# Optimization experiments

Measured on AMD Instinct MI355X. Metric: run time of the kernel, lower is better.

Reference implementation:

```python
import jax, jax.numpy as jnp
import numpy as np

N_NODES = 50000
N_EDGES = 500000
D_FEAT = 128
HIDDEN = 128
EPS = 1e-8


def _lin_init(key, fan_in, fan_out):
    return jax.random.normal(key, (fan_in, fan_out), dtype=jnp.float32) / np.sqrt(fan_in)


def setup_inputs() -> dict:
    key = jax.random.key(0)
    ks = jax.random.split(key, 16)
    h = jax.random.normal(ks[0], (N_NODES, D_FEAT), dtype=jnp.float32)
    coord = jax.random.normal(ks[1], (N_NODES, 3), dtype=jnp.float32)
    vel = jax.random.normal(ks[2], (N_NODES, 3), dtype=jnp.float32)
    edge_index = jax.random.randint(ks[3], (2, N_EDGES), 0, N_NODES, dtype=jnp.int32)
    return {
        "h": h, "coord": coord, "vel": vel, "edge_index": edge_index,
        "W_e1": _lin_init(ks[4], 2 * D_FEAT + 1, HIDDEN), "b_e1": jnp.zeros((HIDDEN,), jnp.float32),
        "W_e2": _lin_init(ks[5], HIDDEN, D_FEAT), "b_e2": jnp.zeros((D_FEAT,), jnp.float32),
        "W_c1": _lin_init(ks[6], D_FEAT, HIDDEN), "b_c1": jnp.zeros((HIDDEN,), jnp.float32),
        "W_c2": _lin_init(ks[7], HIDDEN, 1), "b_c2": jnp.zeros((1,), jnp.float32),
        "W_v1": _lin_init(ks[8], D_FEAT, HIDDEN), "b_v1": jnp.zeros((HIDDEN,), jnp.float32),
        "W_v2": _lin_init(ks[9], HIDDEN, 1), "b_v2": jnp.zeros((1,), jnp.float32),
        "W_n1": _lin_init(ks[10], 2 * D_FEAT, HIDDEN), "b_n1": jnp.zeros((HIDDEN,), jnp.float32),
        "W_n2": _lin_init(ks[11], HIDDEN, D_FEAT), "b_n2": jnp.zeros((D_FEAT,), jnp.float32),
    }


def reference(h, coord, vel, edge_index,
              W_e1, b_e1, W_e2, b_e2,
              W_c1, b_c1, W_c2, b_c2,
              W_v1, b_v1, W_v2, b_v2,
              W_n1, b_n1, W_n2, b_n2):
    act = jax.nn.silu
    r, c = edge_index[0], edge_index[1]
    n = coord.shape[0]

    # coord2radial with normalize=True
    diff = coord[r] - coord[c]                      # [E, 3]
    rad = jnp.sum(diff * diff, axis=-1, keepdims=True)  # [E, 1]
    norm = jnp.sqrt(jax.lax.stop_gradient(rad)) + EPS
    diff = diff / norm

    # edge_op: Linear -> act -> Linear -> act
    edge_in = jnp.concatenate([h[r], h[c], rad], axis=1)  # [E, 2D+1]
    m_ij = act(act(edge_in @ W_e1 + b_e1) @ W_e2 + b_e2)  # [E, D]

    # coord_op: Linear -> act -> Linear (scalar weight per edge)
    weights = act(m_ij @ W_c1 + b_c1) @ W_c2 + b_c2       # [E, 1]
    coors_sum = jax.ops.segment_sum(diff * weights, r, num_segments=n)  # [N, 3]

    # vel_op: Linear -> act -> Linear (scalar per node)
    vel_weights = act(h @ W_v1 + b_v1) @ W_v2 + b_v2      # [N, 1]
    coord_out = coord + coors_sum + vel * vel_weights

    # node aggregation + node_op: Linear -> act -> Linear
    m_i = jax.ops.segment_sum(m_ij, r, num_segments=h.shape[0])  # [N, D]
    agg = jnp.concatenate([h, m_i], axis=1)               # [N, 2D]
    h_out = act(agg @ W_n1 + b_n1) @ W_n2 + b_n2          # [N, D]
    return (h_out, coord_out)
```

## Files before the change

kernel.cpp:

```cpp
#include <hip/hip_runtime.h>
#include <stdint.h>

#define NN 50000
#define NE 500000
#define BLK 256
#define NEB ((NE + 127) / 128)
#define SST 136

#define BARRIER() asm volatile("s_waitcnt lgkmcnt(0)\n\ts_barrier" ::: "memory")

typedef __attribute__((ext_vector_type(8))) short bf16x8;
typedef __attribute__((ext_vector_type(4))) float f32x4;

__device__ __forceinline__ float silu(float x) { return x / (1.0f + __expf(-x)); }
__device__ __forceinline__ float bf2f(unsigned short s) {
    union { unsigned int u; float f; } v; v.u = ((unsigned int)s) << 16; return v.f;
}
__device__ __forceinline__ unsigned short f2bf(float f) {
    union { float f; unsigned int u; } v; v.f = f;
    return (unsigned short)((v.u + 0x7fffu + ((v.u >> 16) & 1u)) >> 16);
}
__device__ __forceinline__ unsigned int pack2(float a, float b) {
    unsigned int r;
    asm("v_cvt_pk_bf16_f32 %0, %1, %2" : "=v"(r) : "v"(a), "v"(b));
    return r;
}
__device__ __forceinline__ bf16x8 packf8(const float* p) {
    float4 f0 = *(const float4*)p; float4 f1 = *(const float4*)(p + 4);
    union { bf16x8 v; unsigned int u[4]; } o;
    o.u[0] = pack2(f0.x, f0.y); o.u[1] = pack2(f0.z, f0.w);
    o.u[2] = pack2(f1.x, f1.y); o.u[3] = pack2(f1.z, f1.w);
    return o.v;
}

__global__ void prep_h(const float* __restrict__ h, unsigned short* __restrict__ hb) {
    int i = blockIdx.x * 256 + threadIdx.x;
    if (i < NN * 128 / 4) {
        float4 v = ((const float4*)h)[i];
        uint2 o; o.x = pack2(v.x, v.y); o.y = pack2(v.z, v.w);
        ((uint2*)hb)[i] = o;
    }
}

__global__ void prep_w(const float* __restrict__ We1, const float* __restrict__ We2,
                       const float* __restrict__ Wc1, const float* __restrict__ Wv1,
                       const float* __restrict__ Wn1, const float* __restrict__ Wn2,
                       unsigned short* __restrict__ Wt1, unsigned short* __restrict__ Wt2,
                       unsigned short* __restrict__ Wt3, unsigned short* __restrict__ Wv1t,
                       unsigned short* __restrict__ Wn1t, unsigned short* __restrict__ Wn2t) {
    int i = blockIdx.x * 256 + threadIdx.x;
    if (i < 32768) {
        int j = i >> 8, k = i & 255;
        Wt1[i] = f2bf(We1[k * 128 + j]);
    } else if (i < 49152) {
        int t = i - 32768; int j = t >> 7, ks = t & 127;
        int k0 = (ks & 7) * 16 + (ks >> 3);
        Wt2[t] = f2bf(We2[k0 * 128 + j]);
    } else if (i < 65536) {
        int t = i - 49152; int j = t >> 7, ks = t & 127;
        int k0 = (ks & 7) * 16 + (ks >> 3);
        Wt3[t] = f2bf(Wc1[k0 * 128 + j]);
    } else if (i < 81920) {
        int t = i - 65536; int j = t >> 7, k = t & 127;
        Wv1t[t] = f2bf(Wv1[k * 128 + j]);
    } else if (i < 114688) {
        int t = i - 81920; int j = t >> 8, k = t & 255;
        int ksrc;
        if (k < 128) ksrc = k;
        else { int ks = k - 128; ksrc = 128 + (ks & 7) * 16 + (ks >> 3); }
        Wn1t[t] = f2bf(Wn1[ksrc * 128 + j]);
    } else if (i < 131072) {
        int t = i - 114688; int j = t >> 7, ks = t & 127;
        int k0 = (ks & 7) * 16 + (ks >> 3);
        Wn2t[t] = f2bf(Wn2[k0 * 128 + j]);
    }
}

__global__ void csr_count(const int* __restrict__ eidx, int* __restrict__ deg) {
    int e = blockIdx.x * 256 + threadIdx.x;
    if (e < NE) atomicAdd(&deg[eidx[e]], 1);
}

__global__ void scan_a(const int* __restrict__ deg, int* __restrict__ bsum) {
    __shared__ int s[256];
    int t = threadIdx.x, idx = blockIdx.x * 256 + t;
    s[t] = (idx < NN) ? deg[idx] : 0;
    __syncthreads();
    for (int off = 128; off > 0; off >>= 1) {
        if (t < off) s[t] += s[t + off];
        __syncthreads();
    }
    if (t == 0) bsum[blockIdx.x] = s[0];
}

__global__ void scan_b(int* __restrict__ bsum) {
    __shared__ int s[256];
    int t = threadIdx.x;
    int v = (t < 196) ? bsum[t] : 0;
    s[t] = v;
    __syncthreads();
    for (int off = 1; off < 256; off <<= 1) {
        int x = (t >= off) ? s[t - off] : 0;
        __syncthreads();
        s[t] += x;
        __syncthreads();
    }
    if (t < 196) bsum[t] = s[t] - v;
}

__global__ void scan_c(const int* __restrict__ deg, const int* __restrict__ bsum,
                       int* __restrict__ rowptr) {
    __shared__ int s[256];
    int t = threadIdx.x, idx = blockIdx.x * 256 + t;
    int v = (idx < NN) ? deg[idx] : 0;
    s[t] = v;
    __syncthreads();
    for (int off = 1; off < 256; off <<= 1) {
        int x = (t >= off) ? s[t - off] : 0;
        __syncthreads();
        s[t] += x;
        __syncthreads();
    }
    if (idx < NN) rowptr[idx] = bsum[blockIdx.x] + s[t] - v;
    if (idx == 0) rowptr[NN] = NE;
}

__global__ void csr_fill(const int* __restrict__ eidx, const int* __restrict__ rowptr,
                         int* __restrict__ cursor,
                         int* __restrict__ csr_r, int* __restrict__ csr_c) {
    int e = blockIdx.x * 256 + threadIdx.x;
    if (e < NE) {
        int r = eidx[e], c = eidx[NE + e];
        int slot = rowptr[r] + atomicAdd(&cursor[r], 1);
        csr_r[slot] = r; csr_c[slot] = c;
    }
}

__device__ __forceinline__ void wpref256(const unsigned short* __restrict__ W, int halfk,
                                         uint4 w[8], int tid) {
#pragma unroll
    for (int t = 0; t < 8; ++t) {
        int idx = tid + t * 256; int j = idx >> 4, g = idx & 15;
        w[t] = *(const uint4*)(W + (size_t)j * 256 + halfk * 128 + g * 8);
    }
}
__device__ __forceinline__ void wpref128(const unsigned short* __restrict__ W,
                                         uint4 w[8], int tid) {
#pragma unroll
    for (int t = 0; t < 8; ++t) {
        int idx = tid + t * 256; int j = idx >> 4, g = idx & 15;
        w[t] = *(const uint4*)(W + (size_t)j * 128 + g * 8);
    }
}
__device__ __forceinline__ void wwrite(const uint4 w[8], unsigned short* sW, int tid) {
#pragma unroll
    for (int t = 0; t < 8; ++t) {
        int idx = tid + t * 256; int j = idx >> 4, g = idx & 15;
        *(uint4*)(sW + j * SST + g * 8) = w[t];
    }
}
__device__ __forceinline__ void mfma4(const bf16x8 a[2][4], const unsigned short* sW,
                                      int l16, int q, f32x4 acc[2][8]) {
#pragma unroll
    for (int kc = 0; kc < 4; ++kc)
#pragma unroll
        for (int ct = 0; ct < 8; ++ct) {
            bf16x8 b = *(const bf16x8*)(sW + (ct * 16 + l16) * SST + kc * 32 + q * 8);
            acc[0][ct] = __builtin_amdgcn_mfma_f32_16x16x32_bf16(a[0][kc], b, acc[0][ct], 0, 0, 0);
            acc[1][ct] = __builtin_amdgcn_mfma_f32_16x16x32_bf16(a[1][kc], b, acc[1][ct], 0, 0, 0);
        }
}

__global__ __launch_bounds__(BLK, 2) void egcl_edge(
    const float* __restrict__ coord,
    const int* __restrict__ csr_r, const int* __restrict__ csr_c,
    const unsigned short* __restrict__ hb,
    const unsigned short* __restrict__ Wt1,
    const unsigned short* __restrict__ Wt2,
    const unsigned short* __restrict__ Wt3,
    const float* __restrict__ We1,
    const float* __restrict__ be1, const float* __restrict__ be2,
    const float* __restrict__ bc1,
    const float* __restrict__ Wc2, const float* __restrict__ bc2,
    float* __restrict__ m_acc, float* __restrict__ c_sum)
{
    __shared__ __align__(16) unsigned short sAb[128 * SST];
    __shared__ __align__(16) unsigned short sW[128 * SST];
    __shared__ float sRad[128], sDif[128][3];
    __shared__ int sSeg[128];
    __shared__ float sBe1[128], sBe2[128], sBc1[128], sWlast[128], sWc2f[128];

    const int tid = threadIdx.x;
    const int wv = tid >> 6, lane = tid & 63, q = lane >> 4, l16 = lane & 15;
    const int e0 = blockIdx.x * 128;

    int nr[2], nc[2];
#pragma unroll
    for (int si = 0; si < 2; ++si) {
        int e = e0 + (wv * 2 + si) * 16 + l16;
        if (e >= NE) e = NE - 1;
        nr[si] = csr_r[e]; nc[si] = csr_c[e];
    }

    if (tid < 128) {
        sBe1[tid] = be1[tid]; sBe2[tid] = be2[tid]; sBc1[tid] = bc1[tid];
        sWlast[tid] = We1[256 * 128 + tid]; sWc2f[tid] = Wc2[tid];
        int s = e0 + tid; int sc = (s < NE) ? s : (NE - 1);
        int r = csr_r[sc], c = csr_c[sc];
        sSeg[tid] = (s < NE) ? r : -1;
        float dx = coord[r * 3 + 0] - coord[c * 3 + 0];
        float dy = coord[r * 3 + 1] - coord[c * 3 + 1];
        float dz = coord[r * 3 + 2] - coord[c * 3 + 2];
        float rad = fmaf(dx, dx, fmaf(dy, dy, dz * dz));
        float inv = 1.0f / (sqrtf(rad) + 1e-8f);
        sRad[tid] = rad;
        sDif[tid][0] = dx * inv; sDif[tid][1] = dy * inv; sDif[tid][2] = dz * inv;
    }

    uint4 wA[8], wB[8];
    wpref256(Wt1, 0, wA, tid);
    wpref256(Wt1, 1, wB, tid);
    bf16x8 ar[2][4], ac[2][4];
#pragma unroll
    for (int si = 0; si < 2; ++si)
#pragma unroll
        for (int kc = 0; kc < 4; ++kc) {
            ar[si][kc] = *(const bf16x8*)(hb + (size_t)nr[si] * 128 + kc * 32 + q * 8);
            ac[si][kc] = *(const bf16x8*)(hb + (size_t)nc[si] * 128 + kc * 32 + q * 8);
        }
    wwrite(wA, sW, tid);
    wwrite(wB, sAb, tid);
    wpref128(Wt2, wA, tid);
    const float bc2v = bc2[0];
    BARRIER();

    f32x4 acc[2][8];
#pragma unroll
    for (int si = 0; si < 2; ++si)
#pragma unroll
        for (int ct = 0; ct < 8; ++ct) acc[si][ct] = (f32x4){0.f, 0.f, 0.f, 0.f};

    mfma4(ar, sW, l16, q, acc);
    mfma4(ac, sAb, l16, q, acc);
    BARRIER();
    wwrite(wA, sW, tid);
    wpref128(Wt3, wA, tid);

#pragma unroll
    for (int si = 0; si < 2; ++si)
#pragma unroll
        for (int r = 0; r < 4; ++r) {
            int row = (wv * 2 + si) * 16 + q * 4 + r;
            float rad = sRad[row];
            float v[8];
#pragma unroll
            for (int ct = 0; ct < 8; ++ct) {
                int col = ct * 16 + l16;
                v[ct] = silu(acc[si][ct][r] + rad * sWlast[col] + sBe1[col]);
            }
            uint4 pk = make_uint4(pack2(v[0], v[1]), pack2(v[2], v[3]),
                                  pack2(v[4], v[5]), pack2(v[6], v[7]));
            *(uint4*)(sAb + row * SST + l16 * 8) = pk;
        }
    BARRIER();

#pragma unroll
    for (int si = 0; si < 2; ++si)
#pragma unroll
        for (int ct = 0; ct < 8; ++ct) acc[si][ct] = (f32x4){0.f, 0.f, 0.f, 0.f};
    {
        bf16x8 a[2][4];
#pragma unroll
        for (int si = 0; si < 2; ++si) {
            int row = (wv * 2 + si) * 16 + l16;
#pragma unroll
            for (int kc = 0; kc < 4; ++kc)
                a[si][kc] = *(const bf16x8*)(sAb + row * SST + kc * 32 + q * 8);
        }
        mfma4(a, sW, l16, q, acc);
    }
#pragma unroll
    for (int si = 0; si < 2; ++si)
#pragma unroll
        for (int r = 0; r < 4; ++r) {
            float v[8];
#pragma unroll
            for (int ct = 0; ct < 8; ++ct) v[ct] = silu(acc[si][ct][r] + sBe2[ct * 16 + l16]);
            int row = (wv * 2 + si) * 16 + q * 4 + r;
            *(uint4*)(sAb + row * SST + l16 * 8) =
                make_uint4(pack2(v[0], v[1]), pack2(v[2], v[3]),
                           pack2(v[4], v[5]), pack2(v[6], v[7]));
        }
    BARRIER();
    wwrite(wA, sW, tid);
    BARRIER();

#pragma unroll
    for (int si = 0; si < 2; ++si)
#pragma unroll
        for (int ct = 0; ct < 8; ++ct) acc[si][ct] = (f32x4){0.f, 0.f, 0.f, 0.f};
    {
        bf16x8 a[2][4];
#pragma unroll
        for (int si = 0; si < 2; ++si) {
            int row = (wv * 2 + si) * 16 + l16;
#pragma unroll
            for (int kc = 0; kc < 4; ++kc)
                a[si][kc] = *(const bf16x8*)(sAb + row * SST + kc * 32 + q * 8);
        }
        mfma4(a, sW, l16, q, acc);
    }
#pragma unroll
    for (int si = 0; si < 2; ++si) {
        float p[4];
#pragma unroll
        for (int r = 0; r < 4; ++r) {
            float s = 0.f;
#pragma unroll
            for (int ct = 0; ct < 8; ++ct) {
                int col = ct * 16 + l16;
                float t = silu(acc[si][ct][r] + sBc1[col]);
                s = fmaf(t, sWc2f[col], s);
            }
            p[r] = s;
        }
#pragma unroll
        for (int m = 1; m < 16; m <<= 1)
#pragma unroll
            for (int r = 0; r < 4; ++r) p[r] += __shfl_xor(p[r], m, 16);
        if (l16 == 0) {
#pragma unroll
            for (int r = 0; r < 4; ++r) {
                int row = (wv * 2 + si) * 16 + q * 4 + r;
                int rn = sSeg[row];
                if (rn >= 0) {
                    float wgt = p[r] + bc2v;
                    atomicAdd(&c_sum[(size_t)rn * 3 + 0], sDif[row][0] * wgt);
                    atomicAdd(&c_sum[(size_t)rn * 3 + 1], sDif[row][1] * wgt);
                    atomicAdd(&c_sum[(size_t)rn * 3 + 2], sDif[row][2] * wgt);
                }
            }
        }
    }

    {
        int p = tid & 127, half = tid >> 7;
        int base = half * 64;
        float run = 0.f;
        int cur = sSeg[base];
        bool openL = true;
#pragma unroll 1
        for (int i0 = 0; i0 < 64; i0 += 4) {
            float v[4]; int rr[4];
#pragma unroll
            for (int j = 0; j < 4; ++j) {
                int row = base + i0 + j;
                rr[j] = sSeg[row];
                v[j] = bf2f(sAb[row * SST + p]);
            }
#pragma unroll
            for (int j = 0; j < 4; ++j) {
                if (rr[j] != cur) {
                    if (cur >= 0) {
                        float* dst = &m_acc[(size_t)cur * 128 + p];
                        if (openL) atomicAdd(dst, run);
                        else       *dst = run;
                    }
                    run = 0.f; cur = rr[j]; openL = false;
                }
                run += v[j];
            }
        }
        if (cur >= 0) atomicAdd(&m_acc[(size_t)cur * 128 + p], run);
    }
}

__global__ __launch_bounds__(BLK, 3) void egcl_node(
    const unsigned short* __restrict__ hb,
    const float* __restrict__ coord,
    const float* __restrict__ vel,
    const unsigned short* __restrict__ Wv1t, const float* __restrict__ bv1,
    const float* __restrict__ Wv2, const float* __restrict__ bv2,
    const unsigned short* __restrict__ Wn1t, const float* __restrict__ bn1,
    const unsigned short* __restrict__ Wn2t, const float* __restrict__ bn2,
    const float* __restrict__ m_acc, const float* __restrict__ c_sum,
    float* __restrict__ out_h, float* __restrict__ out_c)
{
    __shared__ __align__(16) unsigned short sAb[128 * SST];
    __shared__ float sBv1[128], sWv2f[128], sBn1[128], sBn2[128];

    const int tid = threadIdx.x;
    const int wv = tid >> 6, lane = tid & 63, q = lane >> 4, l16 = lane & 15;
    const int n0 = blockIdx.x * 128;
    int nval = NN - n0; if (nval > 128) nval = 128;

    if (tid < 128) {
        sBv1[tid] = bv1[tid]; sWv2f[tid] = Wv2[tid];
        sBn1[tid] = bn1[tid]; sBn2[tid] = bn2[tid];
    }
    const float bv2v = bv2[0];

    bf16x8 ah[2][4], am[2][4];
#pragma unroll
    for (int si = 0; si < 2; ++si) {
        int row = (wv * 2 + si) * 16 + l16;
        int nn = n0 + row; if (nn >= NN) nn = NN - 1;
#pragma unroll
        for (int kc = 0; kc < 4; ++kc) {
            ah[si][kc] = *(const bf16x8*)(hb + (size_t)nn * 128 + kc * 32 + q * 8);
            am[si][kc] = packf8(m_acc + (size_t)nn * 128 + kc * 32 + q * 8);
        }
    }

    BARRIER();

    f32x4 acc[2][8];
#pragma unroll
    for (int si = 0; si < 2; ++si)
#pragma unroll
        for (int ct = 0; ct < 8; ++ct) acc[si][ct] = (f32x4){0.f, 0.f, 0.f, 0.f};
#pragma unroll
    for (int kc = 0; kc < 4; ++kc)
#pragma unroll
        for (int ct = 0; ct < 8; ++ct) {
            bf16x8 b = *(const bf16x8*)(Wv1t + (size_t)(ct * 16 + l16) * 128 + kc * 32 + q * 8);
            acc[0][ct] = __builtin_amdgcn_mfma_f32_16x16x32_bf16(ah[0][kc], b, acc[0][ct], 0, 0, 0);
            acc[1][ct] = __builtin_amdgcn_mfma_f32_16x16x32_bf16(ah[1][kc], b, acc[1][ct], 0, 0, 0);
        }
#pragma unroll
    for (int si = 0; si < 2; ++si) {
        float p[4];
#pragma unroll
        for (int r = 0; r < 4; ++r) {
            float s = 0.f;
#pragma unroll
            for (int ct = 0; ct < 8; ++ct) {
                int col = ct * 16 + l16;
                float t = silu(acc[si][ct][r] + sBv1[col]);
                s = fmaf(t, sWv2f[col], s);
            }
            p[r] = s;
        }
#pragma unroll
        for (int m = 1; m < 16; m <<= 1)
#pragma unroll
            for (int r = 0; r < 4; ++r) p[r] += __shfl_xor(p[r], m, 16);
        if (l16 == 0) {
#pragma unroll
            for (int r = 0; r < 4; ++r) {
                int row = (wv * 2 + si) * 16 + q * 4 + r;
                int n = n0 + row;
                if (row < nval) {
                    float vw = p[r] + bv2v;
#pragma unroll
                    for (int d = 0; d < 3; ++d) {
                        float cv = coord[(size_t)n * 3 + d] + c_sum[(size_t)n * 3 + d]
                                 + vel[(size_t)n * 3 + d] * vw;
                        out_c[(size_t)n * 3 + d] = cv;
                    }
                }
            }
        }
    }

#pragma unroll
    for (int si = 0; si < 2; ++si)
#pragma unroll
        for (int ct = 0; ct < 8; ++ct) acc[si][ct] = (f32x4){0.f, 0.f, 0.f, 0.f};
#pragma unroll
    for (int kc = 0; kc < 8; ++kc)
#pragma unroll
        for (int ct = 0; ct < 8; ++ct) {
            bf16x8 b = *(const bf16x8*)(Wn1t + (size_t)(ct * 16 + l16) * 256 + kc * 32 + q * 8);
            bf16x8 a0 = (kc < 4) ? ah[0][kc & 3] : am[0][kc & 3];
            bf16x8 a1 = (kc < 4) ? ah[1][kc & 3] : am[1][kc & 3];
            acc[0][ct] = __builtin_amdgcn_mfma_f32_16x16x32_bf16(a0, b, acc[0][ct], 0, 0, 0);
            acc[1][ct] = __builtin_amdgcn_mfma_f32_16x16x32_bf16(a1, b, acc[1][ct], 0, 0, 0);
        }
#pragma unroll
    for (int si = 0; si < 2; ++si)
#pragma unroll
        for (int r = 0; r < 4; ++r) {
            int row = (wv * 2 + si) * 16 + q * 4 + r;
            float v[8];
#pragma unroll
            for (int ct = 0; ct < 8; ++ct) v[ct] = silu(acc[si][ct][r] + sBn1[ct * 16 + l16]);
            uint4 pk = make_uint4(pack2(v[0], v[1]), pack2(v[2], v[3]),
                                  pack2(v[4], v[5]), pack2(v[6], v[7]));
            *(uint4*)(sAb + row * SST + l16 * 8) = pk;
        }

    BARRIER();

#pragma unroll
    for (int si = 0; si < 2; ++si)
#pragma unroll
        for (int ct = 0; ct < 8; ++ct) acc[si][ct] = (f32x4){0.f, 0.f, 0.f, 0.f};
    {
        bf16x8 a[2][4];
#pragma unroll
        for (int si = 0; si < 2; ++si) {
            int row = (wv * 2 + si) * 16 + l16;
#pragma unroll
            for (int kc = 0; kc < 4; ++kc)
                a[si][kc] = *(const bf16x8*)(sAb + row * SST + kc * 32 + q * 8);
        }
#pragma unroll
        for (int kc = 0; kc < 4; ++kc)
#pragma unroll
            for (int ct = 0; ct < 8; ++ct) {
                bf16x8 b = *(const bf16x8*)(Wn2t + (size_t)(ct * 16 + l16) * 128 + kc * 32 + q * 8);
                acc[0][ct] = __builtin_amdgcn_mfma_f32_16x16x32_bf16(a[0][kc], b, acc[0][ct], 0, 0, 0);
                acc[1][ct] = __builtin_amdgcn_mfma_f32_16x16x32_bf16(a[1][kc], b, acc[1][ct], 0, 0, 0);
            }
    }
#pragma unroll
    for (int si = 0; si < 2; ++si)
#pragma unroll
        for (int r = 0; r < 4; ++r) {
            int row = (wv * 2 + si) * 16 + q * 4 + r;
            if (row < nval) {
                float* orow = out_h + (size_t)(n0 + row) * 128;
#pragma unroll
                for (int ct = 0; ct < 8; ++ct)
                    orow[ct * 16 + l16] = acc[si][ct][r] + sBn2[ct * 16 + l16];
            }
        }
}

extern "C" void kernel_launch(void* const* d_in, const int* in_sizes, int n_in,
                              void* d_out, int out_size, void* d_ws, size_t ws_size,
                              hipStream_t stream) {
    const float* h     = (const float*)d_in[0];
    const float* coord = (const float*)d_in[1];
    const float* vel   = (const float*)d_in[2];
    const int*   eidx  = (const int*)d_in[3];
    const float* We1 = (const float*)d_in[4];
    const float* be1 = (const float*)d_in[5];
    const float* We2 = (const float*)d_in[6];
    const float* be2 = (const float*)d_in[7];
    const float* Wc1 = (const float*)d_in[8];
    const float* bc1 = (const float*)d_in[9];
    const float* Wc2 = (const float*)d_in[10];
    const float* bc2 = (const float*)d_in[11];
    const float* Wv1 = (const float*)d_in[12];
    const float* bv1 = (const float*)d_in[13];
    const float* Wv2 = (const float*)d_in[14];
    const float* bv2 = (const float*)d_in[15];
    const float* Wn1 = (const float*)d_in[16];
    const float* bn1 = (const float*)d_in[17];
    const float* Wn2 = (const float*)d_in[18];
    const float* bn2 = (const float*)d_in[19];

    char* ws = (char*)d_ws;
    float* m_acc = (float*)ws;
    float* c_sum = (float*)(ws + 25600000);
    unsigned short* hb   = (unsigned short*)(ws + 26200064);
    unsigned short* Wt1  = (unsigned short*)(ws + 39000064);
    unsigned short* Wt2  = (unsigned short*)(ws + 39065600);
    unsigned short* Wt3  = (unsigned short*)(ws + 39098368);
    unsigned short* Wv1t = (unsigned short*)(ws + 39131136);
    unsigned short* Wn1t = (unsigned short*)(ws + 39163904);
    unsigned short* Wn2t = (unsigned short*)(ws + 39229440);
    int* deg    = (int*)(ws + 39262208);
    int* cursor = (int*)(ws + 39462208);
    int* rowptr = (int*)(ws + 39662208);
    int* bsum   = (int*)(ws + 39862272);
    int* csr_r  = (int*)(ws + 39863296);
    int* csr_c  = (int*)(ws + 41863296);

    hipMemsetAsync(ws, 0, 26200000, stream);
    hipMemsetAsync(ws + 39262208, 0, 400000, stream);

    prep_h<<<6250, 256, 0, stream>>>(h, hb);
    prep_w<<<512, 256, 0, stream>>>(We1, We2, Wc1, Wv1, Wn1, Wn2,
                                    Wt1, Wt2, Wt3, Wv1t, Wn1t, Wn2t);

    csr_count<<<1954, 256, 0, stream>>>(eidx, deg);
    scan_a<<<196, 256, 0, stream>>>(deg, bsum);
    scan_b<<<1, 256, 0, stream>>>(bsum);
    scan_c<<<196, 256, 0, stream>>>(deg, bsum, rowptr);
    csr_fill<<<1954, 256, 0, stream>>>(eidx, rowptr, cursor, csr_r, csr_c);

    egcl_edge<<<NEB, BLK, 0, stream>>>(
        coord, csr_r, csr_c, hb, Wt1, Wt2, Wt3,
        We1, be1, be2, bc1, Wc2, bc2, m_acc, c_sum);

    float* out_h = (float*)d_out;
    float* out_c = out_h + (size_t)NN * 128;
    egcl_node<<<(NN + 127) / 128, BLK, 0, stream>>>(
        hb, coord, vel, Wv1t, bv1, Wv2, bv2, Wn1t, bn1, Wn2t, bn2,
        m_acc, c_sum, out_h, out_c);
}
```

Measured before the change: 414.5 us.

## Fuse prep kernels, reuse degree counters, and halve per-wave tiles in edge/node kernels

Merges the h conversion, weight transposition, degree counting and workspace zeroing into one prep launch, replacing two memsets and three kernels. The cursor array goes away because csr_fill now decrements the degree counters to assign slots. The edge kernel moves to 512-thread blocks where each wave handles 16 edges instead of 32, and the node kernel uses 64-node tiles; both cut register use so more waves fit per CU. The node kernel also drops a block barrier in favour of an LDS wait, which is safe only because each wave reads back just its own rows. Trade-offs: more weight-staging traffic per edge, and a reversed slot order within each CSR row.

Result: slower. 427.3 us (+3.1%).

```diff
diff --git a/kernel.cpp b/kernel.cpp
--- a/kernel.cpp
+++ b/kernel.cpp
@@ -3,11 +3,12 @@
 
 #define NN 50000
 #define NE 500000
-#define BLK 256
+#define EBLK 512
 #define NEB ((NE + 127) / 128)
 #define SST 136
 
 #define BARRIER() asm volatile("s_waitcnt lgkmcnt(0)\n\ts_barrier" ::: "memory")
+#define LGKM0() asm volatile("s_waitcnt lgkmcnt(0)" ::: "memory")
 
 typedef __attribute__((ext_vector_type(8))) short bf16x8;
 typedef __attribute__((ext_vector_type(4))) float f32x4;
@@ -33,52 +34,55 @@
     return o.v;
 }
 
-__global__ void prep_h(const float* __restrict__ h, unsigned short* __restrict__ hb) {
-    int i = blockIdx.x * 256 + threadIdx.x;
-    if (i < NN * 128 / 4) {
+__global__ void prep_all(const float* __restrict__ h, unsigned short* __restrict__ hb,
+                         const float* __restrict__ We1, const float* __restrict__ We2,
+                         const float* __restrict__ Wc1, const float* __restrict__ Wv1,
+                         const float* __restrict__ Wn1, const float* __restrict__ Wn2,
+                         unsigned short* __restrict__ Wt1, unsigned short* __restrict__ Wt2,
+                         unsigned short* __restrict__ Wt3, unsigned short* __restrict__ Wv1t,
+                         unsigned short* __restrict__ Wn1t, unsigned short* __restrict__ Wn2t,
+                         const int* __restrict__ eidx, int* __restrict__ deg,
+                         float4* __restrict__ zbase) {
+    int b = blockIdx.x, tid = threadIdx.x;
+    if (b < 6250) {
+        int i = b * 256 + tid;
         float4 v = ((const float4*)h)[i];
         uint2 o; o.x = pack2(v.x, v.y); o.y = pack2(v.z, v.w);
         ((uint2*)hb)[i] = o;
-    }
-}
-
-__global__ void prep_w(const float* __restrict__ We1, const float* __restrict__ We2,
-                       const float* __restrict__ Wc1, const float* __restrict__ Wv1,
-                       const float* __restrict__ Wn1, const float* __restrict__ Wn2,
-                       unsigned short* __restrict__ Wt1, unsigned short* __restrict__ Wt2,
-                       unsigned short* __restrict__ Wt3, unsigned short* __restrict__ Wv1t,
-                       unsigned short* __restrict__ Wn1t, unsigned short* __restrict__ Wn2t) {
-    int i = blockIdx.x * 256 + threadIdx.x;
-    if (i < 32768) {
-        int j = i >> 8, k = i & 255;
-        Wt1[i] = f2bf(We1[k * 128 + j]);
-    } else if (i < 49152) {
-        int t = i - 32768; int j = t >> 7, ks = t & 127;
-        int k0 = (ks & 7) * 16 + (ks >> 3);
-        Wt2[t] = f2bf(We2[k0 * 128 + j]);
-    } else if (i < 65536) {
-        int t = i - 49152; int j = t >> 7, ks = t & 127;
-        int k0 = (ks & 7) * 16 + (ks >> 3);
-        Wt3[t] = f2bf(Wc1[k0 * 128 + j]);
-    } else if (i < 81920) {
-        int t = i - 65536; int j = t >> 7, k = t & 127;
-        Wv1t[t] = f2bf(Wv1[k * 128 + j]);
-    } else if (i < 114688) {
-        int t = i - 81920; int j = t >> 8, k = t & 255;
-        int ksrc;
-        if (k < 128) ksrc = k;
-        else { int ks = k - 128; ksrc = 128 + (ks & 7) * 16 + (ks >> 3); }
-        Wn1t[t] = f2bf(Wn1[ksrc * 128 + j]);
-    } else if (i < 131072) {
-        int t = i - 114688; int j = t >> 7, ks = t & 127;
-        int k0 = (ks & 7) * 16 + (ks >> 3);
-        Wn2t[t] = f2bf(Wn2[k0 * 128 + j]);
-    }
-}
-
-__global__ void csr_count(const int* __restrict__ eidx, int* __restrict__ deg) {
-    int e = blockIdx.x * 256 + threadIdx.x;
-    if (e < NE) atomicAdd(&deg[eidx[e]], 1);
+    } else if (b < 6762) {
+        int i = (b - 6250) * 256 + tid;
+        if (i < 32768) {
+            int j = i >> 8, k = i & 255;
+            Wt1[i] = f2bf(We1[k * 128 + j]);
+        } else if (i < 49152) {
+            int t = i - 32768; int j = t >> 7, ks = t & 127;
+            int k0 = (ks & 7) * 16 + (ks >> 3);
+            Wt2[t] = f2bf(We2[k0 * 128 + j]);
+        } else if (i < 65536) {
+            int t = i - 49152; int j = t >> 7, ks = t & 127;
+            int k0 = (ks & 7) * 16 + (ks >> 3);
+            Wt3[t] = f2bf(Wc1[k0 * 128 + j]);
+        } else if (i < 81920) {
+            int t = i - 65536; int j = t >> 7, k = t & 127;
+            Wv1t[t] = f2bf(Wv1[k * 128 + j]);
+        } else if (i < 114688) {
+            int t = i - 81920; int j = t >> 8, k = t & 255;
+            int ksrc;
+            if (k < 128) ksrc = k;
+            else { int ks = k - 128; ksrc = 128 + (ks & 7) * 16 + (ks >> 3); }
+            Wn1t[t] = f2bf(Wn1[ksrc * 128 + j]);
+        } else if (i < 131072) {
+            int t = i - 114688; int j = t >> 7, ks = t & 127;
+            int k0 = (ks & 7) * 16 + (ks >> 3);
+            Wn2t[t] = f2bf(Wn2[k0 * 128 + j]);
+        }
+    } else if (b < 8716) {
+        int e = (b - 6762) * 256 + tid;
+        if (e < NE) atomicAdd(&deg[eidx[e]], 1);
+    } else {
+        int i = (b - 8716) * 256 + tid;
+        if (i < 1637500) zbase[i] = make_float4(0.f, 0.f, 0.f, 0.f);
+    }
 }
 
 __global__ void scan_a(const int* __restrict__ deg, int* __restrict__ bsum) {
@@ -126,52 +130,51 @@
 }
 
 __global__ void csr_fill(const int* __restrict__ eidx, const int* __restrict__ rowptr,
-                         int* __restrict__ cursor,
+                         int* __restrict__ deg,
                          int* __restrict__ csr_r, int* __restrict__ csr_c) {
     int e = blockIdx.x * 256 + threadIdx.x;
     if (e < NE) {
         int r = eidx[e], c = eidx[NE + e];
-        int slot = rowptr[r] + atomicAdd(&cursor[r], 1);
+        int slot = rowptr[r] + atomicSub(&deg[r], 1) - 1;
         csr_r[slot] = r; csr_c[slot] = c;
     }
 }
 
 __device__ __forceinline__ void wpref256(const unsigned short* __restrict__ W, int halfk,
-                                         uint4 w[8], int tid) {
-#pragma unroll
-    for (int t = 0; t < 8; ++t) {
-        int idx = tid + t * 256; int j = idx >> 4, g = idx & 15;
+                                         uint4 w[4], int tid) {
+#pragma unroll
+    for (int t = 0; t < 4; ++t) {
+        int idx = tid + t * 512; int j = idx >> 4, g = idx & 15;
         w[t] = *(const uint4*)(W + (size_t)j * 256 + halfk * 128 + g * 8);
     }
 }
 __device__ __forceinline__ void wpref128(const unsigned short* __restrict__ W,
-                                         uint4 w[8], int tid) {
-#pragma unroll
-    for (int t = 0; t < 8; ++t) {
-        int idx = tid + t * 256; int j = idx >> 4, g = idx & 15;
+                                         uint4 w[4], int tid) {
+#pragma unroll
+    for (int t = 0; t < 4; ++t) {
+        int idx = tid + t * 512; int j = idx >> 4, g = idx & 15;
         w[t] = *(const uint4*)(W + (size_t)j * 128 + g * 8);
     }
 }
-__device__ __forceinline__ void wwrite(const uint4 w[8], unsigned short* sW, int tid) {
-#pragma unroll
-    for (int t = 0; t < 8; ++t) {
-        int idx = tid + t * 256; int j = idx >> 4, g = idx & 15;
+__device__ __forceinline__ void wwrite(const uint4 w[4], unsigned short* sW, int tid) {
+#pragma unroll
+    for (int t = 0; t < 4; ++t) {
+        int idx = tid + t * 512; int j = idx >> 4, g = idx & 15;
         *(uint4*)(sW + j * SST + g * 8) = w[t];
     }
 }
-__device__ __forceinline__ void mfma4(const bf16x8 a[2][4], const unsigned short* sW,
-                                      int l16, int q, f32x4 acc[2][8]) {
+__device__ __forceinline__ void mfma4(const bf16x8 a[4], const unsigned short* sW,
+                                      int l16, int q, f32x4 acc[8]) {
 #pragma unroll
     for (int kc = 0; kc < 4; ++kc)
 #pragma unroll
         for (int ct = 0; ct < 8; ++ct) {
             bf16x8 b = *(const bf16x8*)(sW + (ct * 16 + l16) * SST + kc * 32 + q * 8);
-            acc[0][ct] = __builtin_amdgcn_mfma_f32_16x16x32_bf16(a[0][kc], b, acc[0][ct], 0, 0, 0);
-            acc[1][ct] = __builtin_amdgcn_mfma_f32_16x16x32_bf16(a[1][kc], b, acc[1][ct], 0, 0, 0);
-        }
-}
-
-__global__ __launch_bounds__(BLK, 2) void egcl_edge(
+            acc[ct] = __builtin_amdgcn_mfma_f32_16x16x32_bf16(a[kc], b, acc[ct], 0, 0, 0);
+        }
+}
+
+__global__ __launch_bounds__(EBLK, 4) void egcl_edge(
     const float* __restrict__ coord,
     const int* __restrict__ csr_r, const int* __restrict__ csr_c,
     const unsigned short* __restrict__ hb,
@@ -194,13 +197,9 @@
     const int wv = tid >> 6, lane = tid & 63, q = lane >> 4, l16 = lane & 15;
     const int e0 = blockIdx.x * 128;
 
-    int nr[2], nc[2];
-#pragma unroll
-    for (int si = 0; si < 2; ++si) {
-        int e = e0 + (wv * 2 + si) * 16 + l16;
-        if (e >= NE) e = NE - 1;
-        nr[si] = csr_r[e]; nc[si] = csr_c[e];
-    }
+    int er = e0 + wv * 16 + l16;
+    if (er >= NE) er = NE - 1;
+    const int nr = csr_r[er], nc = csr_c[er];
 
     if (tid < 128) {
         sBe1[tid] = be1[tid]; sBe2[tid] = be2[tid]; sBc1[tid] = bc1[tid];
@@ -217,28 +216,24 @@
         sDif[tid][0] = dx * inv; sDif[tid][1] = dy * inv; sDif[tid][2] = dz * inv;
     }
 
-    uint4 wA[8], wB[8];
+    uint4 wA[4], wB[4];
     wpref256(Wt1, 0, wA, tid);
     wpref256(Wt1, 1, wB, tid);
-    bf16x8 ar[2][4], ac[2][4];
-#pragma unroll
-    for (int si = 0; si < 2; ++si)
-#pragma unroll
-        for (int kc = 0; kc < 4; ++kc) {
-            ar[si][kc] = *(const bf16x8*)(hb + (size_t)nr[si] * 128 + kc * 32 + q * 8);
-            ac[si][kc] = *(const bf16x8*)(hb + (size_t)nc[si] * 128 + kc * 32 + q * 8);
-        }
+    bf16x8 ar[4], ac[4];
+#pragma unroll
+    for (int kc = 0; kc < 4; ++kc) {
+        ar[kc] = *(const bf16x8*)(hb + (size_t)nr * 128 + kc * 32 + q * 8);
+        ac[kc] = *(const bf16x8*)(hb + (size_t)nc * 128 + kc * 32 + q * 8);
+    }
     wwrite(wA, sW, tid);
     wwrite(wB, sAb, tid);
     wpref128(Wt2, wA, tid);
     const float bc2v = bc2[0];
     BARRIER();
 
-    f32x4 acc[2][8];
-#pragma unroll
-    for (int si = 0; si < 2; ++si)
-#pragma unroll
-        for (int ct = 0; ct < 8; ++ct) acc[si][ct] = (f32x4){0.f, 0.f, 0.f, 0.f};
+    f32x4 acc[8];
+#pragma unroll
+    for (int ct = 0; ct < 8; ++ct) acc[ct] = (f32x4){0.f, 0.f, 0.f, 0.f};
 
     mfma4(ar, sW, l16, q, acc);
     mfma4(ac, sAb, l16, q, acc);
@@ -247,71 +242,56 @@
     wpref128(Wt3, wA, tid);
 
 #pragma unroll
-    for (int si = 0; si < 2; ++si)
-#pragma unroll
-        for (int r = 0; r < 4; ++r) {
-            int row = (wv * 2 + si) * 16 + q * 4 + r;
-            float rad = sRad[row];
-            float v[8];
-#pragma unroll
-            for (int ct = 0; ct < 8; ++ct) {
-                int col = ct * 16 + l16;
-                v[ct] = silu(acc[si][ct][r] + rad * sWlast[col] + sBe1[col]);
-            }
-            uint4 pk = make_uint4(pack2(v[0], v[1]), pack2(v[2], v[3]),
-                                  pack2(v[4], v[5]), pack2(v[6], v[7]));
-            *(uint4*)(sAb + row * SST + l16 * 8) = pk;
-        }
+    for (int r = 0; r < 4; ++r) {
+        int row = wv * 16 + q * 4 + r;
+        float rad = sRad[row];
+        float v[8];
+#pragma unroll
+        for (int ct = 0; ct < 8; ++ct) {
+            int col = ct * 16 + l16;
+            v[ct] = silu(acc[ct][r] + rad * sWlast[col] + sBe1[col]);
+        }
+        uint4 pk = make_uint4(pack2(v[0], v[1]), pack2(v[2], v[3]),
+                              pack2(v[4], v[5]), pack2(v[6], v[7]));
+        *(uint4*)(sAb + row * SST + l16 * 8) = pk;
+    }
     BARRIER();
 
 #pragma unroll
-    for (int si = 0; si < 2; ++si)
-#pragma unroll
-        for (int ct = 0; ct < 8; ++ct) acc[si][ct] = (f32x4){0.f, 0.f, 0.f, 0.f};
+    for (int ct = 0; ct < 8; ++ct) acc[ct] = (f32x4){0.f, 0.f, 0.f, 0.f};
     {
-        bf16x8 a[2][4];
-#pragma unroll
-        for (int si = 0; si < 2; ++si) {
-            int row = (wv * 2 + si) * 16 + l16;
-#pragma unroll
-            for (int kc = 0; kc < 4; ++kc)
-                a[si][kc] = *(const bf16x8*)(sAb + row * SST + kc * 32 + q * 8);
-        }
+        bf16x8 a[4];
+        int row = wv * 16 + l16;
+#pragma unroll
+        for (int kc = 0; kc < 4; ++kc)
+            a[kc] = *(const bf16x8*)(sAb + row * SST + kc * 32 + q * 8);
         mfma4(a, sW, l16, q, acc);
     }
 #pragma unroll
-    for (int si = 0; si < 2; ++si)
-#pragma unroll
-        for (int r = 0; r < 4; ++r) {
-            float v[8];
-#pragma unroll
-            for (int ct = 0; ct < 8; ++ct) v[ct] = silu(acc[si][ct][r] + sBe2[ct * 16 + l16]);
-            int row = (wv * 2 + si) * 16 + q * 4 + r;
-            *(uint4*)(sAb + row * SST + l16 * 8) =
-                make_uint4(pack2(v[0], v[1]), pack2(v[2], v[3]),
-                           pack2(v[4], v[5]), pack2(v[6], v[7]));
-        }
+    for (int r = 0; r < 4; ++r) {
+        float v[8];
+#pragma unroll
+        for (int ct = 0; ct < 8; ++ct) v[ct] = silu(acc[ct][r] + sBe2[ct * 16 + l16]);
+        int row = wv * 16 + q * 4 + r;
+        *(uint4*)(sAb + row * SST + l16 * 8) =
+            make_uint4(pack2(v[0], v[1]), pack2(v[2], v[3]),
+                       pack2(v[4], v[5]), pack2(v[6], v[7]));
+    }
     BARRIER();
     wwrite(wA, sW, tid);
     BARRIER();
 
 #pragma unroll
-    for (int si = 0; si < 2; ++si)
-#pragma unroll
-        for (int ct = 0; ct < 8; ++ct) acc[si][ct] = (f32x4){0.f, 0.f, 0.f, 0.f};
+    for (int ct = 0; ct < 8; ++ct) acc[ct] = (f32x4){0.f, 0.f, 0.f, 0.f};
     {
-        bf16x8 a[2][4];
-#pragma unroll
-        for (int si = 0; si < 2; ++si) {
-            int row = (wv * 2 + si) * 16 + l16;
-#pragma unroll
-            for (int kc = 0; kc < 4; ++kc)
-                a[si][kc] = *(const bf16x8*)(sAb + row * SST + kc * 32 + q * 8);
-        }
+        bf16x8 a[4];
+        int row = wv * 16 + l16;
+#pragma unroll
+        for (int kc = 0; kc < 4; ++kc)
+            a[kc] = *(const bf16x8*)(sAb + row * SST + kc * 32 + q * 8);
         mfma4(a, sW, l16, q, acc);
     }
-#pragma unroll
-    for (int si = 0; si < 2; ++si) {
+    {
         float p[4];
 #pragma unroll
         for (int r = 0; r < 4; ++r) {
@@ -319,7 +299,7 @@
 #pragma unroll
             for (int ct = 0; ct < 8; ++ct) {
                 int col = ct * 16 + l16;
-                float t = silu(acc[si][ct][r] + sBc1[col]);
+                float t = silu(acc[ct][r] + sBc1[col]);
                 s = fmaf(t, sWc2f[col], s);
             }
             p[r] = s;
@@ -331,7 +311,7 @@
         if (l16 == 0) {
 #pragma unroll
             for (int r = 0; r < 4; ++r) {
-                int row = (wv * 2 + si) * 16 + q * 4 + r;
+                int row = wv * 16 + q * 4 + r;
                 int rn = sSeg[row];
                 if (rn >= 0) {
                     float wgt = p[r] + bc2v;
@@ -343,7 +323,7 @@
         }
     }
 
-    {
+    if (tid < 256) {
         int p = tid & 127, half = tid >> 7;
         int base = half * 64;
         float run = 0.f;
@@ -375,7 +355,7 @@
     }
 }
 
-__global__ __launch_bounds__(BLK, 3) void egcl_node(
+__global__ __launch_bounds__(256, 4) void egcl_node(
     const unsigned short* __restrict__ hb,
     const float* __restrict__ coord,
     const float* __restrict__ vel,
@@ -386,13 +366,13 @@
     const float* __restrict__ m_acc, const float* __restrict__ c_sum,
     float* __restrict__ out_h, float* __restrict__ out_c)
 {
-    __shared__ __align__(16) unsigned short sAb[128 * SST];
+    __shared__ __align__(16) unsigned short sAb[64 * SST];
     __shared__ float sBv1[128], sWv2f[128], sBn1[128], sBn2[128];
 
     const int tid = threadIdx.x;
     const int wv = tid >> 6, lane = tid & 63, q = lane >> 4, l16 = lane & 15;
-    const int n0 = blockIdx.x * 128;
-    int nval = NN - n0; if (nval > 128) nval = 128;
+    const int n0 = blockIdx.x * 64;
+    int nval = NN - n0; if (nval > 64) nval = 64;
 
     if (tid < 128) {
         sBv1[tid] = bv1[tid]; sWv2f[tid] = Wv2[tid];
@@ -400,35 +380,30 @@
     }
     const float bv2v = bv2[0];
 
-    bf16x8 ah[2][4], am[2][4];
-#pragma unroll
-    for (int si = 0; si < 2; ++si) {
-        int row = (wv * 2 + si) * 16 + l16;
+    bf16x8 ah[4], am[4];
+    {
+        int row = wv * 16 + l16;
         int nn = n0 + row; if (nn >= NN) nn = NN - 1;
 #pragma unroll
         for (int kc = 0; kc < 4; ++kc) {
-            ah[si][kc] = *(const bf16x8*)(hb + (size_t)nn * 128 + kc * 32 + q * 8);
-            am[si][kc] = packf8(m_acc + (size_t)nn * 128 + kc * 32 + q * 8);
+            ah[kc] = *(const bf16x8*)(hb + (size_t)nn * 128 + kc * 32 + q * 8);
+            am[kc] = packf8(m_acc + (size_t)nn * 128 + kc * 32 + q * 8);
         }
     }
 
     BARRIER();
 
-    f32x4 acc[2][8];
-#pragma unroll
-    for (int si = 0; si < 2; ++si)
-#pragma unroll
-        for (int ct = 0; ct < 8; ++ct) acc[si][ct] = (f32x4){0.f, 0.f, 0.f, 0.f};
+    f32x4 acc[8];
+#pragma unroll
+    for (int ct = 0; ct < 8; ++ct) acc[ct] = (f32x4){0.f, 0.f, 0.f, 0.f};
 #pragma unroll
     for (int kc = 0; kc < 4; ++kc)
 #pragma unroll
         for (int ct = 0; ct < 8; ++ct) {
             bf16x8 b = *(const bf16x8*)(Wv1t + (size_t)(ct * 16 + l16) * 128 + kc * 32 + q * 8);
-            acc[0][ct] = __builtin_amdgcn_mfma_f32_16x16x32_bf16(ah[0][kc], b, acc[0][ct], 0, 0, 0);
-            acc[1][ct] = __builtin_amdgcn_mfma_f32_16x16x32_bf16(ah[1][kc], b, acc[1][ct], 0, 0, 0);
-        }
-#pragma unroll
-    for (int si = 0; si < 2; ++si) {
+            acc[ct] = __builtin_amdgcn_mfma_f32_16x16x32_bf16(ah[kc], b, acc[ct], 0, 0, 0);
+        }
+    {
         float p[4];
 #pragma unroll
         for (int r = 0; r < 4; ++r) {
@@ -436,7 +411,7 @@
 #pragma unroll
             for (int ct = 0; ct < 8; ++ct) {
                 int col = ct * 16 + l16;
-                float t = silu(acc[si][ct][r] + sBv1[col]);
+                float t = silu(acc[ct][r] + sBv1[col]);
                 s = fmaf(t, sWv2f[col], s);
             }
             p[r] = s;
@@ -448,7 +423,7 @@
         if (l16 == 0) {
 #pragma unroll
             for (int r = 0; r < 4; ++r) {
-                int row = (wv * 2 + si) * 16 + q * 4 + r;
+                int row = wv * 16 + q * 4 + r;
                 int n = n0 + row;
                 if (row < nval) {
                     float vw = p[r] + bv2v;
@@ -464,68 +439,53 @@
     }
 
 #pragma unroll
-    for (int si = 0; si < 2; ++si)
-#pragma unroll
-        for (int ct = 0; ct < 8; ++ct) acc[si][ct] = (f32x4){0.f, 0.f, 0.f, 0.f};
+    for (int ct = 0; ct < 8; ++ct) acc[ct] = (f32x4){0.f, 0.f, 0.f, 0.f};
 #pragma unroll
     for (int kc = 0; kc < 8; ++kc)
 #pragma unroll
         for (int ct = 0; ct < 8; ++ct) {
             bf16x8 b = *(const bf16x8*)(Wn1t + (size_t)(ct * 16 + l16) * 256 + kc * 32 + q * 8);
-            bf16x8 a0 = (kc < 4) ? ah[0][kc & 3] : am[0][kc & 3];
-            bf16x8 a1 = (kc < 4) ? ah[1][kc & 3] : am[1][kc & 3];
-            acc[0][ct] = __builtin_amdgcn_mfma_f32_16x16x32_bf16(a0, b, acc[0][ct], 0, 0, 0);
-            acc[1][ct] = __builtin_amdgcn_mfma_f32_16x16x32_bf16(a1, b, acc[1][ct], 0, 0, 0);
-        }
-#pragma unroll
-    for (int si = 0; si < 2; ++si)
-#pragma unroll
-        for (int r = 0; r < 4; ++r) {
-            int row = (wv * 2 + si) * 16 + q * 4 + r;
-            float v[8];
-#pragma unroll
-            for (int ct = 0; ct < 8; ++ct) v[ct] = silu(acc[si][ct][r] + sBn1[ct * 16 + l16]);
-            uint4 pk = make_uint4(pack2(v[0], v[1]), pack2(v[2], v[3]),
-                                  pack2(v[4], v[5]), pack2(v[6], v[7]));
-            *(uint4*)(sAb + row * SST + l16 * 8) = pk;
-        }
-
-    BARRIER();
-
-#pragma unroll
-    for (int si = 0; si < 2; ++si)
-#pragma unroll
-        for (int ct = 0; ct < 8; ++ct) acc[si][ct] = (f32x4){0.f, 0.f, 0.f, 0.f};
+            bf16x8 a0 = (kc < 4) ? ah[kc & 3] : am[kc & 3];
+            acc[ct] = __builtin_amdgcn_mfma_f32_16x16x32_bf16(a0, b, acc[ct], 0, 0, 0);
+        }
+#pragma unroll
+    for (int r = 0; r < 4; ++r) {
+        int row = wv * 16 + q * 4 + r;
+        float v[8];
+#pragma unroll
+        for (int ct = 0; ct < 8; ++ct) v[ct] = silu(acc[ct][r] + sBn1[ct * 16 + l16]);
+        uint4 pk = make_uint4(pack2(v[0], v[1]), pack2(v[2], v[3]),
+                              pack2(v[4], v[5]), pack2(v[6], v[7]));
+        *(uint4*)(sAb + row * SST + l16 * 8) = pk;
+    }
+    LGKM0();
+
+#pragma unroll
+    for (int ct = 0; ct < 8; ++ct) acc[ct] = (f32x4){0.f, 0.f, 0.f, 0.f};
     {
-        bf16x8 a[2][4];
-#pragma unroll
-        for (int si = 0; si < 2; ++si) {
-            int row = (wv * 2 + si) * 16 + l16;
-#pragma unroll
-            for (int kc = 0; kc < 4; ++kc)
-                a[si][kc] = *(const bf16x8*)(sAb + row * SST + kc * 32 + q * 8);
-        }
+        bf16x8 a[4];
+        int row = wv * 16 + l16;
+#pragma unroll
+        for (int kc = 0; kc < 4; ++kc)
+            a[kc] = *(const bf16x8*)(sAb + row * SST + kc * 32 + q * 8);
 #pragma unroll
         for (int kc = 0; kc < 4; ++kc)
 #pragma unroll
             for (int ct = 0; ct < 8; ++ct) {
                 bf16x8 b = *(const bf16x8*)(Wn2t + (size_t)(ct * 16 + l16) * 128 + kc * 32 + q * 8);
-                acc[0][ct] = __builtin_amdgcn_mfma_f32_16x16x32_bf16(a[0][kc], b, acc[0][ct], 0, 0, 0);
-                acc[1][ct] = __builtin_amdgcn_mfma_f32_16x16x32_bf16(a[1][kc], b, acc[1][ct], 0, 0, 0);
-            }
-    }
-#pragma unroll
-    for (int si = 0; si < 2; ++si)
-#pragma unroll
-        for (int r = 0; r < 4; ++r) {
-            int row = (wv * 2 + si) * 16 + q * 4 + r;
-            if (row < nval) {
-                float* orow = out_h + (size_t)(n0 + row) * 128;
-#pragma unroll
-                for (int ct = 0; ct < 8; ++ct)
-                    orow[ct * 16 + l16] = acc[si][ct][r] + sBn2[ct * 16 + l16];
-            }
-        }
+                acc[ct] = __builtin_amdgcn_mfma_f32_16x16x32_bf16(a[kc], b, acc[ct], 0, 0, 0);
+            }
+    }
+#pragma unroll
+    for (int r = 0; r < 4; ++r) {
+        int row = wv * 16 + q * 4 + r;
+        if (row < nval) {
+            float* orow = out_h + (size_t)(n0 + row) * 128;
+#pragma unroll
+            for (int ct = 0; ct < 8; ++ct)
+                orow[ct * 16 + l16] = acc[ct][r] + sBn2[ct * 16 + l16];
+        }
+    }
 }
 
 extern "C" void kernel_launch(void* const* d_in, const int* in_sizes, int n_in,
@@ -563,32 +523,29 @@
     unsigned short* Wn1t = (unsigned short*)(ws + 39163904);
     unsigned short* Wn2t = (unsigned short*)(ws + 39229440);
     int* deg    = (int*)(ws + 39262208);
-    int* cursor = (int*)(ws + 39462208);
     int* rowptr = (int*)(ws + 39662208);
     int* bsum   = (int*)(ws + 39862272);
     int* csr_r  = (int*)(ws + 39863296);
     int* csr_c  = (int*)(ws + 41863296);
 
-    hipMemsetAsync(ws, 0, 26200000, stream);
-    hipMemsetAsync(ws + 39262208, 0, 400000, stream);
-
-    prep_h<<<6250, 256, 0, stream>>>(h, hb);
-    prep_w<<<512, 256, 0, stream>>>(We1, We2, Wc1, Wv1, Wn1, Wn2,
-                                    Wt1, Wt2, Wt3, Wv1t, Wn1t, Wn2t);
-
-    csr_count<<<1954, 256, 0, stream>>>(eidx, deg);
+    hipMemsetAsync(deg, 0, 200000, stream);
+
+    prep_all<<<15113, 256, 0, stream>>>(h, hb, We1, We2, Wc1, Wv1, Wn1, Wn2,
+                                        Wt1, Wt2, Wt3, Wv1t, Wn1t, Wn2t,
+                                        eidx, deg, (float4*)ws);
+
     scan_a<<<196, 256, 0, stream>>>(deg, bsum);
     scan_b<<<1, 256, 0, stream>>>(bsum);
     scan_c<<<196, 256, 0, stream>>>(deg, bsum, rowptr);
-    csr_fill<<<1954, 256, 0, stream>>>(eidx, rowptr, cursor, csr_r, csr_c);
-
-    egcl_edge<<<NEB, BLK, 0, stream>>>(
+    csr_fill<<<1954, 256, 0, stream>>>(eidx, rowptr, deg, csr_r, csr_c);
+
+    egcl_edge<<<NEB, EBLK, 0, stream>>>(
         coord, csr_r, csr_c, hb, Wt1, Wt2, Wt3,
         We1, be1, be2, bc1, Wc2, bc2, m_acc, c_sum);
 
     float* out_h = (float*)d_out;
     float* out_c = out_h + (size_t)NN * 128;
-    egcl_node<<<(NN + 127) / 128, BLK, 0, stream>>>(
+    egcl_node<<<(NN + 63) / 64, 256, 0, stream>>>(
         hb, coord, vel, Wv1t, bv1, Wv2, bv2, Wn1t, bn1, Wn2t, bn2,
         m_acc, c_sum, out_h, out_c);
 }
```
